# Optimization experiments

Hardware: AMD Instinct MI355X
Metric: run time of the kernel (lower is better)

The kernel has to match this reference:

```python
import jax, jax.numpy as jnp
import numpy as np

NEG_CLAMP = -100.0  # torch F.binary_cross_entropy clamps log terms at -100


def _ccl_labels(fg):
    """4-connectivity connected-component labeling of a [H,W] bool mask.
    Labels are assigned in raster-scan first-encounter order, matching
    scipy.ndimage.label with the default structure. Background = 0.
    Implemented as min-index label propagation to a fixed point: each
    component ends up tagged with the min flat index of its pixels (its
    first raster-scan pixel), then roots are ranked by cumsum to get 1..num.
    """
    H, W = fg.shape
    INF = H * W  # sentinel larger than any flat index
    idx = jnp.arange(INF, dtype=jnp.int32).reshape(H, W)
    init = jnp.where(fg, idx, INF)

    def step(x):
        up = jnp.concatenate([x[1:], jnp.full((1, W), INF, x.dtype)], axis=0)
        down = jnp.concatenate([jnp.full((1, W), INF, x.dtype), x[:-1]], axis=0)
        left = jnp.concatenate([x[:, 1:], jnp.full((H, 1), INF, x.dtype)], axis=1)
        right = jnp.concatenate([jnp.full((H, 1), INF, x.dtype), x[:, :-1]], axis=1)
        m = jnp.minimum(jnp.minimum(up, down), jnp.minimum(left, right))
        return jnp.where(fg, jnp.minimum(x, m), INF)

    def cond(carry):
        return carry[1]

    def body(carry):
        x, _ = carry
        nx = step(x)
        return nx, jnp.any(nx != x)

    x, _ = jax.lax.while_loop(cond, body, (init, jnp.array(True)))

    flat = x.reshape(-1)
    fgf = fg.reshape(-1)
    # a pixel is the root of its component iff its propagated tag == its own index
    is_root = fgf & (flat == jnp.arange(INF, dtype=jnp.int32))
    rank = jnp.cumsum(is_root.astype(jnp.int32))  # rank[r] = scipy label of root r
    labels = jnp.where(fgf, rank[jnp.clip(flat, 0, INF - 1)], 0)
    return labels.reshape(H, W)


def _target_map(fg):
    """Replicates: labels == labels.flatten()[1:].argmax() + 1 (faithful to source,
    including its quirky use of argmax position as the selected label value)."""
    labels = _ccl_labels(fg)
    lf = labels.reshape(-1)
    v = jnp.argmax(lf[1:]) + 1  # first occurrence of max, like numpy argmax
    return (labels == v).astype(jnp.float32)


def setup_inputs() -> dict:
    key = jax.random.key(0)
    pred = jax.random.uniform(key, (32, 1, 512, 512), dtype=jnp.float32)
    return {"pred": pred}


def reference(pred):
    fg = pred[:, 0] >= 0.5  # [N,H,W] bool
    target = jax.vmap(_target_map)(fg)[:, None]  # [N,1,H,W] float
    logp = jnp.maximum(jnp.log(pred), NEG_CLAMP)
    log1mp = jnp.maximum(jnp.log1p(-pred), NEG_CLAMP)
    return -jnp.mean(target * logp + (1.0 - target) * log1mp)
```

## Files before the change

### kernel.cpp

```cpp
#include <hip/hip_runtime.h>
#include <math.h>

#define IMG_W 512
#define IMG_H 512
#define HW (IMG_W * IMG_H)
#define LOGHW 18
#define NIMG 32
#define NTOT (NIMG * HW)
#define TILE 64
#define TPI 64
#define NTILE (NIMG * TPI)
#define CPI 64
#define NSCHUNK (NIMG * CPI)
#define VBORD ((8 - 1) * IMG_H)
#define BORD_PER_IMG (VBORD + (8 - 1) * IMG_W)
#define NBORD (NIMG * BORD_PER_IMG)

__device__ __forceinline__ void uf_unite(int* L, int a, int b) {
    while (true) {
        int p = ((volatile int*)L)[a];
        while (p != a) { a = p; p = ((volatile int*)L)[a]; }
        p = ((volatile int*)L)[b];
        while (p != b) { b = p; p = ((volatile int*)L)[b]; }
        if (a == b) return;
        if (a < b) { int t = a; a = b; b = t; }
        int old = atomicMin(&L[a], b);
        if (old == a) return;
        a = old;
    }
}

__global__ __launch_bounds__(256) void k_local(const float* __restrict__ pred,
                                               int* __restrict__ L,
                                               float* __restrict__ partials) {
    __shared__ int lab[TILE * TILE];
    __shared__ float sred[256];
    int tile = blockIdx.x;
    int img = tile >> 6;
    int t = tile & (TPI - 1);
    int ty = t >> 3, tx = t & 7;
    int baseLocal = (ty * TILE) * IMG_W + tx * TILE;
    const float* pi = pred + ((size_t)img << LOGHW);
    int* Li = L + ((size_t)img << LOGHW);
    int tid = threadIdx.x;
    int lane = tid & 63, wave = tid >> 6;

    float acc = 0.0f;
#pragma unroll
    for (int j = 0; j < 16; j++) {
        int row = wave + j * 4;
        float p = pi[baseLocal + row * IMG_W + lane];
        acc += fmaxf(log1pf(-p), -100.0f);
        bool fg = (p >= 0.5f);
        unsigned long long bal = __ballot(fg);
        unsigned long long starts = bal & ~(bal << 1);
        unsigned long long maskle =
            (lane == 63) ? ~0ULL : ((1ULL << (lane + 1)) - 1ULL);
        int lb = -1;
        if (fg) {
            unsigned long long pre = starts & maskle;
            int startLane = 63 - __builtin_clzll(pre);
            lb = row * TILE + startLane;
        }
        lab[row * TILE + lane] = lb;
    }
    __syncthreads();
#pragma unroll
    for (int j = 0; j < 16; j++) {
        int row = 1 + wave + j * 4;
        if (row > 63) break;
        int i = row * TILE + lane;
        bool c = (lab[i] >= 0) && (lab[i - TILE] >= 0);
        unsigned long long cb = __ballot(c);
        unsigned long long cs = cb & ~(cb << 1);
        if ((cs >> lane) & 1ULL) uf_unite(lab, i, i - TILE);
    }
    __syncthreads();
#pragma unroll
    for (int j = 0; j < 4; j++) {
        int i4 = (tid + j * 256) * 4;
        int ly = i4 >> 6, lx = i4 & 63;
        int4 o;
        int* op = (int*)&o;
#pragma unroll
        for (int k = 0; k < 4; k++) {
            int p = lab[i4 + k];
            if (p < 0) op[k] = -1;
            else {
                int x = i4 + k;
                while (p != x) { x = p; p = lab[x]; }
                op[k] = baseLocal + (x >> 6) * IMG_W + (x & 63);
            }
        }
        *(int4*)(Li + baseLocal + ly * IMG_W + lx) = o;
    }
    sred[tid] = acc;
    __syncthreads();
    for (int s = 128; s > 0; s >>= 1) {
        if (tid < s) sred[tid] += sred[tid + s];
        __syncthreads();
    }
    if (tid == 0) partials[blockIdx.x] = sred[0];
}

__global__ void k_border(int* __restrict__ L) {
    int gid = blockIdx.x * blockDim.x + threadIdx.x;
    if (gid >= NBORD) return;
    int img = gid / BORD_PER_IMG;
    int r = gid - img * BORD_PER_IMG;
    int* Li = L + ((size_t)img << LOGHW);
    int a, b;
    if (r < VBORD) {
        int k = r >> 9, y = r & 511;
        int x = k * TILE + (TILE - 1);
        a = y * IMG_W + x; b = a + 1;
    } else {
        int r2 = r - VBORD;
        int k = r2 >> 9, x = r2 & 511;
        int y = k * TILE + (TILE - 1);
        a = y * IMG_W + x; b = a + IMG_W;
    }
    if (Li[a] >= 0 && Li[b] >= 0) uf_unite(Li, a, b);
}

__global__ __launch_bounds__(256) void k_stats(const int* __restrict__ L,
                                               int* __restrict__ cntArr,
                                               int* __restrict__ maxArr,
                                               int* __restrict__ minArr) {
    __shared__ int s1[256], s2[256], s3[256];
    int chunk = blockIdx.x;
    int img = chunk >> 6;
    int baseL = (chunk & 63) * 4096;
    const int* Li = L + ((size_t)img << LOGHW);
    int t = threadIdx.x;
    int cnt = 0, mx = -1, mn = HW;
#pragma unroll
    for (int j = 0; j < 4; j++) {
        int off = baseL + (t + j * 256) * 4;
        int4 l4 = *(const int4*)(Li + off);
        const int* lp = (const int*)&l4;
#pragma unroll
        for (int k = 0; k < 4; k++) {
            int local = off + k;
            int p = lp[k];
            bool root = (p == local);
            cnt += root ? 1 : 0;
            if (root && local > mx) mx = local;
            if (p >= 0 && local >= 1 && local < mn) mn = local;
        }
    }
    s1[t] = cnt; s2[t] = mx; s3[t] = mn;
    __syncthreads();
    for (int s = 128; s > 0; s >>= 1) {
        if (t < s) {
            s1[t] += s1[t + s];
            s2[t] = max(s2[t], s2[t + s]);
            s3[t] = min(s3[t], s3[t + s]);
        }
        __syncthreads();
    }
    if (t == 0) { cntArr[chunk] = s1[0]; maxArr[chunk] = s2[0]; minArr[chunk] = s3[0]; }
}

__global__ __launch_bounds__(256) void k_rv(const int* __restrict__ cntArr,
                                            const int* __restrict__ maxArr,
                                            const int* __restrict__ minArr,
                                            const int* __restrict__ L,
                                            int* __restrict__ rv) {
    __shared__ int sc[256], sm[256], sn[256];
    __shared__ int sel_chunk, sel_base, result;
    int img = blockIdx.x, t = threadIdx.x;
    int cnt = (t < CPI) ? cntArr[img * CPI + t] : 0;
    sc[t] = cnt;
    sm[t] = (t < CPI) ? maxArr[img * CPI + t] : -1;
    sn[t] = (t < CPI) ? minArr[img * CPI + t] : HW;
    if (t == 0) result = -2;
    __syncthreads();
    for (int off = 1; off < 256; off <<= 1) {
        int v2 = (t >= off) ? sc[t - off] : 0;
        __syncthreads();
        sc[t] += v2;
        __syncthreads();
    }
    int num = sc[255];
    int inc = sc[t], exc = inc - cnt;
    for (int s = 128; s > 0; s >>= 1) {
        if (t < s) { sm[t] = max(sm[t], sm[t + s]); sn[t] = min(sn[t], sn[t + s]); }
        __syncthreads();
    }
    int last_root = sm[0], minFg = sn[0];
    int v;
    if (last_root >= 1) v = last_root;
    else if (last_root == 0) v = (minFg < HW) ? minFg : 1;
    else v = 1;
    if (v >= 1 && v <= num) {
        if (exc < v && v <= inc) { sel_chunk = t; sel_base = exc; }
        __syncthreads();
        int c = sel_chunk, base = sel_base;
        const int* Li = L + ((size_t)img << LOGHW);
        int baseL = c * 4096;
        int f[16];
        int sum = 0;
#pragma unroll
        for (int j = 0; j < 4; j++) {
            int off = baseL + t * 16 + j * 4;
            int4 l4 = *(const int4*)(Li + off);
            const int* lp = (const int*)&l4;
#pragma unroll
            for (int k = 0; k < 4; k++) {
                f[j * 4 + k] = (lp[k] == off + k) ? 1 : 0;
                sum += f[j * 4 + k];
            }
        }
        __syncthreads();
        sc[t] = sum;
        __syncthreads();
        for (int off = 1; off < 256; off <<= 1) {
            int v2 = (t >= off) ? sc[t - off] : 0;
            __syncthreads();
            sc[t] += v2;
            __syncthreads();
        }
        int exc2 = sc[t] - sum;
        int need = v - base;
        if (exc2 < need && need <= sc[t]) {
            int run = exc2;
#pragma unroll
            for (int k = 0; k < 16; k++) {
                run += f[k];
                if (run == need) { result = baseL + t * 16 + k; break; }
            }
        }
        __syncthreads();
    } else {
        __syncthreads();
    }
    if (t == 0) rv[img] = result;
}

__global__ __launch_bounds__(256) void k_loss(const float* __restrict__ pred,
                                              const int* __restrict__ L,
                                              const int* __restrict__ rvArr,
                                              float* __restrict__ partials2) {
    __shared__ float sred[256];
    int blk = blockIdx.x;
    int img = blk >> 6;
    int rvv = rvArr[img];
    if (rvv < 0) {
        if (threadIdx.x == 0) partials2[blk] = 0.0f;
        return;
    }
    const int* Li = L + ((size_t)img << LOGHW);
    int baseG = blk * 4096;
    int t = threadIdx.x;
    float acc = 0.0f;
#pragma unroll
    for (int j = 0; j < 4; j++) {
        int off = baseG + (t + j * 256) * 4;
        float4 p4 = *(const float4*)(pred + off);
        int4 l4 = *(const int4*)(L + off);
        const float* pp = (const float*)&p4;
        const int* lp = (const int*)&l4;
#pragma unroll
        for (int k = 0; k < 4; k++) {
            int p = lp[k];
            if (p < 0) continue;
            int x = p;
            int q = Li[x];
            while (q != x) { x = q; q = Li[x]; }
            if (x == rvv) {
                float pr = pp[k];
                float logp = fmaxf(logf(pr), -100.0f);
                float log1mp = fmaxf(log1pf(-pr), -100.0f);
                acc += logp - log1mp;
            }
        }
    }
    sred[t] = acc;
    __syncthreads();
    for (int s = 128; s > 0; s >>= 1) {
        if (t < s) sred[t] += sred[t + s];
        __syncthreads();
    }
    if (t == 0) partials2[blk] = sred[0];
}

__global__ __launch_bounds__(256) void k_final(const float* __restrict__ partials,
                                               const float* __restrict__ partials2,
                                               float* __restrict__ out) {
    __shared__ double s[256];
    int t = threadIdx.x;
    double acc = 0.0;
#pragma unroll
    for (int j = 0; j < 8; j++) {
        acc += (double)partials[t + j * 256] + (double)partials2[t + j * 256];
    }
    s[t] = acc;
    __syncthreads();
    for (int st = 128; st > 0; st >>= 1) {
        if (t < st) s[t] += s[t + st];
        __syncthreads();
    }
    if (t == 0) out[0] = (float)(-s[0] / (double)NTOT);
}

extern "C" void kernel_launch(void* const* d_in, const int* in_sizes, int n_in,
                              void* d_out, int out_size, void* d_ws, size_t ws_size,
                              hipStream_t stream) {
    const float* pred = (const float*)d_in[0];
    float* out = (float*)d_out;

    char* ws = (char*)d_ws;
    int* L = (int*)ws;
    int* cntArr = (int*)(ws + (size_t)NTOT * 4);
    int* maxArr = cntArr + NSCHUNK;
    int* minArr = maxArr + NSCHUNK;
    float* partials = (float*)(minArr + NSCHUNK);
    float* partials2 = partials + NTILE;
    int* rv = (int*)(partials2 + NTILE);

    dim3 b(256);
    k_local<<<dim3(NTILE), b, 0, stream>>>(pred, L, partials);
    k_border<<<dim3((NBORD + 255) / 256), b, 0, stream>>>(L);
    k_stats<<<dim3(NSCHUNK), b, 0, stream>>>(L, cntArr, maxArr, minArr);
    k_rv<<<dim3(NIMG), b, 0, stream>>>(cntArr, maxArr, minArr, L, rv);
    k_loss<<<dim3(NTILE), b, 0, stream>>>(pred, L, rv, partials2);
    k_final<<<1, b, 0, stream>>>(partials, partials2, out);
}
```

Baseline: 134.1 us.

## Fuse stats/rv and loss/final via last-block counters, widen local CCL blocks

Merges the per-image root-selection kernel into the stats kernel and the final reduction into the loss kernel, using atomic arrival counters so the last block of each group finishes the work. This removes two kernel launches. k_local now runs 1024 threads per tile and compresses paths in shared memory during root resolution. k_border uses a ballot so only run starts call union. The log terms use fast __logf(1-p) instead of log1pf, which can reduce accuracy near p=0.

```diff
diff --git a/kernel.cpp b/kernel.cpp
--- a/kernel.cpp
+++ b/kernel.cpp
@@ -16,6 +16,9 @@
 #define BORD_PER_IMG (VBORD + (8 - 1) * IMG_W)
 #define NBORD (NIMG * BORD_PER_IMG)
 
+#define AL_ACQ(p) __hip_atomic_load((p), __ATOMIC_ACQUIRE, __HIP_MEMORY_SCOPE_AGENT)
+#define AS_RLX(p, v) __hip_atomic_store((p), (v), __ATOMIC_RELAXED, __HIP_MEMORY_SCOPE_AGENT)
+
 __device__ __forceinline__ void uf_unite(int* L, int a, int b) {
     while (true) {
         int p = ((volatile int*)L)[a];
@@ -30,11 +33,12 @@
     }
 }
 
-__global__ __launch_bounds__(256) void k_local(const float* __restrict__ pred,
-                                               int* __restrict__ L,
-                                               float* __restrict__ partials) {
+__global__ __launch_bounds__(1024) void k_local(const float* __restrict__ pred,
+                                                int* __restrict__ L,
+                                                float* __restrict__ partials,
+                                                unsigned int* __restrict__ counters) {
     __shared__ int lab[TILE * TILE];
-    __shared__ float sred[256];
+    __shared__ float sred[1024];
     int tile = blockIdx.x;
     int img = tile >> 6;
     int t = tile & (TPI - 1);
@@ -47,10 +51,10 @@
 
     float acc = 0.0f;
 #pragma unroll
-    for (int j = 0; j < 16; j++) {
-        int row = wave + j * 4;
+    for (int j = 0; j < 4; j++) {
+        int row = wave + j * 16;
         float p = pi[baseLocal + row * IMG_W + lane];
-        acc += fmaxf(log1pf(-p), -100.0f);
+        acc += fmaxf(__logf(1.0f - p), -100.0f);
         bool fg = (p >= 0.5f);
         unsigned long long bal = __ballot(fg);
         unsigned long long starts = bal & ~(bal << 1);
@@ -59,16 +63,15 @@
         int lb = -1;
         if (fg) {
             unsigned long long pre = starts & maskle;
-            int startLane = 63 - __builtin_clzll(pre);
-            lb = row * TILE + startLane;
+            lb = row * TILE + (63 - __builtin_clzll(pre));
         }
         lab[row * TILE + lane] = lb;
     }
     __syncthreads();
 #pragma unroll
-    for (int j = 0; j < 16; j++) {
-        int row = 1 + wave + j * 4;
-        if (row > 63) break;
+    for (int j = 0; j < 4; j++) {
+        int row = wave + j * 16;
+        if (row == 0) continue;
         int i = row * TILE + lane;
         bool c = (lab[i] >= 0) && (lab[i - TILE] >= 0);
         unsigned long long cb = __ballot(c);
@@ -76,19 +79,23 @@
         if ((cs >> lane) & 1ULL) uf_unite(lab, i, i - TILE);
     }
     __syncthreads();
-#pragma unroll
-    for (int j = 0; j < 4; j++) {
-        int i4 = (tid + j * 256) * 4;
+    {
+        int i4 = tid * 4;
         int ly = i4 >> 6, lx = i4 & 63;
         int4 o;
         int* op = (int*)&o;
 #pragma unroll
         for (int k = 0; k < 4; k++) {
-            int p = lab[i4 + k];
+            int x = i4 + k;
+            int p = lab[x];
             if (p < 0) op[k] = -1;
             else {
-                int x = i4 + k;
-                while (p != x) { x = p; p = lab[x]; }
+                while (p != x) {
+                    int g = lab[p];
+                    lab[x] = g;
+                    x = g;
+                    p = lab[x];
+                }
                 op[k] = baseLocal + (x >> 6) * IMG_W + (x & 63);
             }
         }
@@ -96,16 +103,16 @@
     }
     sred[tid] = acc;
     __syncthreads();
-    for (int s = 128; s > 0; s >>= 1) {
+    for (int s = 512; s > 0; s >>= 1) {
         if (tid < s) sred[tid] += sred[tid + s];
         __syncthreads();
     }
     if (tid == 0) partials[blockIdx.x] = sred[0];
+    if (blockIdx.x == 0 && tid <= NIMG) counters[tid] = 0u;
 }
 
 __global__ void k_border(int* __restrict__ L) {
     int gid = blockIdx.x * blockDim.x + threadIdx.x;
-    if (gid >= NBORD) return;
     int img = gid / BORD_PER_IMG;
     int r = gid - img * BORD_PER_IMG;
     int* Li = L + ((size_t)img << LOGHW);
@@ -120,14 +127,21 @@
         int y = k * TILE + (TILE - 1);
         a = y * IMG_W + x; b = a + IMG_W;
     }
-    if (Li[a] >= 0 && Li[b] >= 0) uf_unite(Li, a, b);
-}
-
-__global__ __launch_bounds__(256) void k_stats(const int* __restrict__ L,
-                                               int* __restrict__ cntArr,
-                                               int* __restrict__ maxArr,
-                                               int* __restrict__ minArr) {
+    bool c = (Li[a] >= 0) && (Li[b] >= 0);
+    unsigned long long cb = __ballot(c);
+    unsigned long long cs = cb & ~(cb << 1);
+    if ((cs >> (threadIdx.x & 63)) & 1ULL) uf_unite(Li, a, b);
+}
+
+__global__ __launch_bounds__(256) void k_stats_rv(const int* __restrict__ L,
+                                                  int* __restrict__ cntArr,
+                                                  int* __restrict__ maxArr,
+                                                  int* __restrict__ minArr,
+                                                  unsigned int* __restrict__ counters,
+                                                  int* __restrict__ rv) {
     __shared__ int s1[256], s2[256], s3[256];
+    __shared__ int sel_chunk, sel_base, result;
+    __shared__ unsigned int oldc;
     int chunk = blockIdx.x;
     int img = chunk >> 6;
     int baseL = (chunk & 63) * 4096;
@@ -159,36 +173,35 @@
         }
         __syncthreads();
     }
-    if (t == 0) { cntArr[chunk] = s1[0]; maxArr[chunk] = s2[0]; minArr[chunk] = s3[0]; }
-}
-
-__global__ __launch_bounds__(256) void k_rv(const int* __restrict__ cntArr,
-                                            const int* __restrict__ maxArr,
-                                            const int* __restrict__ minArr,
-                                            const int* __restrict__ L,
-                                            int* __restrict__ rv) {
-    __shared__ int sc[256], sm[256], sn[256];
-    __shared__ int sel_chunk, sel_base, result;
-    int img = blockIdx.x, t = threadIdx.x;
-    int cnt = (t < CPI) ? cntArr[img * CPI + t] : 0;
-    sc[t] = cnt;
-    sm[t] = (t < CPI) ? maxArr[img * CPI + t] : -1;
-    sn[t] = (t < CPI) ? minArr[img * CPI + t] : HW;
+    if (t == 0) {
+        AS_RLX(&cntArr[chunk], s1[0]);
+        AS_RLX(&maxArr[chunk], s2[0]);
+        AS_RLX(&minArr[chunk], s3[0]);
+        oldc = __hip_atomic_fetch_add(&counters[img], 1u,
+                                      __ATOMIC_ACQ_REL, __HIP_MEMORY_SCOPE_AGENT);
+    }
+    __syncthreads();
+    if (oldc != CPI - 1) return;
+
+    int c0 = (t < CPI) ? AL_ACQ(&cntArr[img * CPI + t]) : 0;
+    s1[t] = c0;
+    s2[t] = (t < CPI) ? AL_ACQ(&maxArr[img * CPI + t]) : -1;
+    s3[t] = (t < CPI) ? AL_ACQ(&minArr[img * CPI + t]) : HW;
     if (t == 0) result = -2;
     __syncthreads();
     for (int off = 1; off < 256; off <<= 1) {
-        int v2 = (t >= off) ? sc[t - off] : 0;
-        __syncthreads();
-        sc[t] += v2;
-        __syncthreads();
-    }
-    int num = sc[255];
-    int inc = sc[t], exc = inc - cnt;
+        int v2 = (t >= off) ? s1[t - off] : 0;
+        __syncthreads();
+        s1[t] += v2;
+        __syncthreads();
+    }
+    int num = s1[255];
+    int inc = s1[t], exc = inc - c0;
     for (int s = 128; s > 0; s >>= 1) {
-        if (t < s) { sm[t] = max(sm[t], sm[t + s]); sn[t] = min(sn[t], sn[t + s]); }
-        __syncthreads();
-    }
-    int last_root = sm[0], minFg = sn[0];
+        if (t < s) { s2[t] = max(s2[t], s2[t + s]); s3[t] = min(s3[t], s3[t + s]); }
+        __syncthreads();
+    }
+    int last_root = s2[0], minFg = s3[0];
     int v;
     if (last_root >= 1) v = last_root;
     else if (last_root == 0) v = (minFg < HW) ? minFg : 1;
@@ -197,13 +210,12 @@
         if (exc < v && v <= inc) { sel_chunk = t; sel_base = exc; }
         __syncthreads();
         int c = sel_chunk, base = sel_base;
-        const int* Li = L + ((size_t)img << LOGHW);
-        int baseL = c * 4096;
+        int bL = c * 4096;
         int f[16];
         int sum = 0;
 #pragma unroll
         for (int j = 0; j < 4; j++) {
-            int off = baseL + t * 16 + j * 4;
+            int off = bL + t * 16 + j * 4;
             int4 l4 = *(const int4*)(Li + off);
             const int* lp = (const int*)&l4;
 #pragma unroll
@@ -213,22 +225,22 @@
             }
         }
         __syncthreads();
-        sc[t] = sum;
+        s1[t] = sum;
         __syncthreads();
         for (int off = 1; off < 256; off <<= 1) {
-            int v2 = (t >= off) ? sc[t - off] : 0;
+            int v2 = (t >= off) ? s1[t - off] : 0;
             __syncthreads();
-            sc[t] += v2;
+            s1[t] += v2;
             __syncthreads();
         }
-        int exc2 = sc[t] - sum;
+        int exc2 = s1[t] - sum;
         int need = v - base;
-        if (exc2 < need && need <= sc[t]) {
+        if (exc2 < need && need <= s1[t]) {
             int run = exc2;
 #pragma unroll
             for (int k = 0; k < 16; k++) {
                 run += f[k];
-                if (run == need) { result = baseL + t * 16 + k; break; }
+                if (run == need) { result = bL + t * 16 + k; break; }
             }
         }
         __syncthreads();
@@ -241,67 +253,71 @@
 __global__ __launch_bounds__(256) void k_loss(const float* __restrict__ pred,
                                               const int* __restrict__ L,
                                               const int* __restrict__ rvArr,
-                                              float* __restrict__ partials2) {
+                                              const float* __restrict__ partials,
+                                              float* __restrict__ partials2,
+                                              unsigned int* __restrict__ counters,
+                                              float* __restrict__ out) {
     __shared__ float sred[256];
+    __shared__ double sd[256];
+    __shared__ unsigned int oldc;
     int blk = blockIdx.x;
     int img = blk >> 6;
+    int t = threadIdx.x;
     int rvv = rvArr[img];
-    if (rvv < 0) {
-        if (threadIdx.x == 0) partials2[blk] = 0.0f;
-        return;
-    }
-    const int* Li = L + ((size_t)img << LOGHW);
-    int baseG = blk * 4096;
-    int t = threadIdx.x;
-    float acc = 0.0f;
-#pragma unroll
-    for (int j = 0; j < 4; j++) {
-        int off = baseG + (t + j * 256) * 4;
-        float4 p4 = *(const float4*)(pred + off);
-        int4 l4 = *(const int4*)(L + off);
-        const float* pp = (const float*)&p4;
-        const int* lp = (const int*)&l4;
-#pragma unroll
-        for (int k = 0; k < 4; k++) {
-            int p = lp[k];
-            if (p < 0) continue;
-            int x = p;
-            int q = Li[x];
-            while (q != x) { x = q; q = Li[x]; }
-            if (x == rvv) {
-                float pr = pp[k];
-                float logp = fmaxf(logf(pr), -100.0f);
-                float log1mp = fmaxf(log1pf(-pr), -100.0f);
-                acc += logp - log1mp;
+    float blocksum = 0.0f;
+    if (rvv >= 0) {
+        const int* Li = L + ((size_t)img << LOGHW);
+        int baseG = blk * 4096;
+        float acc = 0.0f;
+#pragma unroll
+        for (int j = 0; j < 4; j++) {
+            int off = baseG + (t + j * 256) * 4;
+            float4 p4 = *(const float4*)(pred + off);
+            int4 l4 = *(const int4*)(L + off);
+            const float* pp = (const float*)&p4;
+            const int* lp = (const int*)&l4;
+#pragma unroll
+            for (int k = 0; k < 4; k++) {
+                int p = lp[k];
+                if (p < 0) continue;
+                int x = p, q = Li[x];
+                while (q != x) { x = q; q = Li[x]; }
+                if (x == rvv) {
+                    float pr = pp[k];
+                    acc += fmaxf(__logf(pr), -100.0f)
+                         - fmaxf(__logf(1.0f - pr), -100.0f);
+                }
             }
         }
-    }
-    sred[t] = acc;
+        sred[t] = acc;
+        __syncthreads();
+        for (int s = 128; s > 0; s >>= 1) {
+            if (t < s) sred[t] += sred[t + s];
+            __syncthreads();
+        }
+        blocksum = sred[0];
+    }
+    if (t == 0) {
+        AS_RLX(&partials2[blk], blocksum);
+        oldc = __hip_atomic_fetch_add(&counters[NIMG], 1u,
+                                      __ATOMIC_ACQ_REL, __HIP_MEMORY_SCOPE_AGENT);
+    }
+    __syncthreads();
+    if (oldc != NTILE - 1) return;
+
+    double acc = 0.0;
+#pragma unroll
+    for (int j = 0; j < 8; j++) {
+        int idx = t + j * 256;
+        acc += (double)partials[idx] + (double)AL_ACQ(&partials2[idx]);
+    }
+    sd[t] = acc;
     __syncthreads();
     for (int s = 128; s > 0; s >>= 1) {
-        if (t < s) sred[t] += sred[t + s];
-        __syncthreads();
-    }
-    if (t == 0) partials2[blk] = sred[0];
-}
-
-__global__ __launch_bounds__(256) void k_final(const float* __restrict__ partials,
-                                               const float* __restrict__ partials2,
-                                               float* __restrict__ out) {
-    __shared__ double s[256];
-    int t = threadIdx.x;
-    double acc = 0.0;
-#pragma unroll
-    for (int j = 0; j < 8; j++) {
-        acc += (double)partials[t + j * 256] + (double)partials2[t + j * 256];
-    }
-    s[t] = acc;
-    __syncthreads();
-    for (int st = 128; st > 0; st >>= 1) {
-        if (t < st) s[t] += s[t + st];
-        __syncthreads();
-    }
-    if (t == 0) out[0] = (float)(-s[0] / (double)NTOT);
+        if (t < s) sd[t] += sd[t + s];
+        __syncthreads();
+    }
+    if (t == 0) out[0] = (float)(-sd[0] / (double)NTOT);
 }
 
 extern "C" void kernel_launch(void* const* d_in, const int* in_sizes, int n_in,
@@ -318,12 +334,12 @@
     float* partials = (float*)(minArr + NSCHUNK);
     float* partials2 = partials + NTILE;
     int* rv = (int*)(partials2 + NTILE);
-
-    dim3 b(256);
-    k_local<<<dim3(NTILE), b, 0, stream>>>(pred, L, partials);
-    k_border<<<dim3((NBORD + 255) / 256), b, 0, stream>>>(L);
-    k_stats<<<dim3(NSCHUNK), b, 0, stream>>>(L, cntArr, maxArr, minArr);
-    k_rv<<<dim3(NIMG), b, 0, stream>>>(cntArr, maxArr, minArr, L, rv);
-    k_loss<<<dim3(NTILE), b, 0, stream>>>(pred, L, rv, partials2);
-    k_final<<<1, b, 0, stream>>>(partials, partials2, out);
-}
+    unsigned int* counters = (unsigned int*)(rv + NIMG);
+
+    k_local<<<dim3(NTILE), dim3(1024), 0, stream>>>(pred, L, partials, counters);
+    k_border<<<dim3(NBORD / 256), dim3(256), 0, stream>>>(L);
+    k_stats_rv<<<dim3(NSCHUNK), dim3(256), 0, stream>>>(L, cntArr, maxArr, minArr,
+                                                        counters, rv);
+    k_loss<<<dim3(NTILE), dim3(256), 0, stream>>>(pred, L, rv, partials, partials2,
+                                                  counters, out);
+}
```

Result: slower. 223.9 us (+66.9%).

## Widen local CCL blocks, use fast logs, compress paths, dedupe border unions

Applied to the files above, without the earlier changes.

The local labeling kernel now runs with 512 threads per tile, so each wave handles fewer rows. Root-finding in shared memory gains path compression. Exact log1pf/logf calls are replaced by the __logf intrinsic on 1-p, which is cheaper but less accurate for p near 0 or 1. The border kernel drops its bounds check and uses a wave ballot so only the first pixel of each contiguous run of joinable pairs performs a union, cutting atomic traffic at the cost of relying on the run structure for correctness.

```diff
diff --git a/kernel.cpp b/kernel.cpp
--- a/kernel.cpp
+++ b/kernel.cpp
@@ -16,6 +16,7 @@
 #define BORD_PER_IMG (VBORD + (8 - 1) * IMG_W)
 #define NBORD (NIMG * BORD_PER_IMG)
 
+
 __device__ __forceinline__ void uf_unite(int* L, int a, int b) {
     while (true) {
         int p = ((volatile int*)L)[a];
@@ -30,11 +31,11 @@
     }
 }
 
-__global__ __launch_bounds__(256) void k_local(const float* __restrict__ pred,
+__global__ __launch_bounds__(512) void k_local(const float* __restrict__ pred,
                                                int* __restrict__ L,
                                                float* __restrict__ partials) {
     __shared__ int lab[TILE * TILE];
-    __shared__ float sred[256];
+    __shared__ float sred[512];
     int tile = blockIdx.x;
     int img = tile >> 6;
     int t = tile & (TPI - 1);
@@ -47,10 +48,10 @@
 
     float acc = 0.0f;
 #pragma unroll
-    for (int j = 0; j < 16; j++) {
-        int row = wave + j * 4;
+    for (int j = 0; j < 8; j++) {
+        int row = wave + j * 8;
         float p = pi[baseLocal + row * IMG_W + lane];
-        acc += fmaxf(log1pf(-p), -100.0f);
+        acc += fmaxf(__logf(1.0f - p), -100.0f);
         bool fg = (p >= 0.5f);
         unsigned long long bal = __ballot(fg);
         unsigned long long starts = bal & ~(bal << 1);
@@ -59,16 +60,15 @@
         int lb = -1;
         if (fg) {
             unsigned long long pre = starts & maskle;
-            int startLane = 63 - __builtin_clzll(pre);
-            lb = row * TILE + startLane;
+            lb = row * TILE + (63 - __builtin_clzll(pre));
         }
         lab[row * TILE + lane] = lb;
     }
     __syncthreads();
 #pragma unroll
-    for (int j = 0; j < 16; j++) {
-        int row = 1 + wave + j * 4;
-        if (row > 63) break;
+    for (int j = 0; j < 8; j++) {
+        int row = wave + j * 8;
+        if (row == 0) continue;
         int i = row * TILE + lane;
         bool c = (lab[i] >= 0) && (lab[i - TILE] >= 0);
         unsigned long long cb = __ballot(c);
@@ -77,18 +77,23 @@
     }
     __syncthreads();
 #pragma unroll
-    for (int j = 0; j < 4; j++) {
-        int i4 = (tid + j * 256) * 4;
+    for (int j = 0; j < 2; j++) {
+        int i4 = (tid + j * 512) * 4;
         int ly = i4 >> 6, lx = i4 & 63;
         int4 o;
         int* op = (int*)&o;
 #pragma unroll
         for (int k = 0; k < 4; k++) {
-            int p = lab[i4 + k];
+            int x = i4 + k;
+            int p = lab[x];
             if (p < 0) op[k] = -1;
             else {
-                int x = i4 + k;
-                while (p != x) { x = p; p = lab[x]; }
+                while (p != x) {
+                    int g = lab[p];
+                    lab[x] = g;
+                    x = g;
+                    p = lab[x];
+                }
                 op[k] = baseLocal + (x >> 6) * IMG_W + (x & 63);
             }
         }
@@ -96,7 +101,7 @@
     }
     sred[tid] = acc;
     __syncthreads();
-    for (int s = 128; s > 0; s >>= 1) {
+    for (int s = 256; s > 0; s >>= 1) {
         if (tid < s) sred[tid] += sred[tid + s];
         __syncthreads();
     }
@@ -105,7 +110,6 @@
 
 __global__ void k_border(int* __restrict__ L) {
     int gid = blockIdx.x * blockDim.x + threadIdx.x;
-    if (gid >= NBORD) return;
     int img = gid / BORD_PER_IMG;
     int r = gid - img * BORD_PER_IMG;
     int* Li = L + ((size_t)img << LOGHW);
@@ -120,7 +124,10 @@
         int y = k * TILE + (TILE - 1);
         a = y * IMG_W + x; b = a + IMG_W;
     }
-    if (Li[a] >= 0 && Li[b] >= 0) uf_unite(Li, a, b);
+    bool c = (Li[a] >= 0) && (Li[b] >= 0);
+    unsigned long long cb = __ballot(c);
+    unsigned long long cs = cb & ~(cb << 1);
+    if ((cs >> (threadIdx.x & 63)) & 1ULL) uf_unite(Li, a, b);
 }
 
 __global__ __launch_bounds__(256) void k_stats(const int* __restrict__ L,
@@ -245,14 +252,14 @@
     __shared__ float sred[256];
     int blk = blockIdx.x;
     int img = blk >> 6;
+    int t = threadIdx.x;
     int rvv = rvArr[img];
     if (rvv < 0) {
-        if (threadIdx.x == 0) partials2[blk] = 0.0f;
+        if (t == 0) partials2[blk] = 0.0f;
         return;
     }
     const int* Li = L + ((size_t)img << LOGHW);
     int baseG = blk * 4096;
-    int t = threadIdx.x;
     float acc = 0.0f;
 #pragma unroll
     for (int j = 0; j < 4; j++) {
@@ -265,14 +272,12 @@
         for (int k = 0; k < 4; k++) {
             int p = lp[k];
             if (p < 0) continue;
-            int x = p;
-            int q = Li[x];
+            int x = p, q = Li[x];
             while (q != x) { x = q; q = Li[x]; }
             if (x == rvv) {
                 float pr = pp[k];
-                float logp = fmaxf(logf(pr), -100.0f);
-                float log1mp = fmaxf(log1pf(-pr), -100.0f);
-                acc += logp - log1mp;
+                acc += fmaxf(__logf(pr), -100.0f)
+                     - fmaxf(__logf(1.0f - pr), -100.0f);
             }
         }
     }
@@ -293,7 +298,8 @@
     double acc = 0.0;
 #pragma unroll
     for (int j = 0; j < 8; j++) {
-        acc += (double)partials[t + j * 256] + (double)partials2[t + j * 256];
+        int idx = t + j * 256;
+        acc += (double)partials[idx] + (double)partials2[idx];
     }
     s[t] = acc;
     __syncthreads();
@@ -317,13 +323,12 @@
     int* minArr = maxArr + NSCHUNK;
     float* partials = (float*)(minArr + NSCHUNK);
     float* partials2 = partials + NTILE;
-    int* rv = (int*)(partials2 + NTILE);
-
-    dim3 b(256);
-    k_local<<<dim3(NTILE), b, 0, stream>>>(pred, L, partials);
-    k_border<<<dim3((NBORD + 255) / 256), b, 0, stream>>>(L);
-    k_stats<<<dim3(NSCHUNK), b, 0, stream>>>(L, cntArr, maxArr, minArr);
-    k_rv<<<dim3(NIMG), b, 0, stream>>>(cntArr, maxArr, minArr, L, rv);
-    k_loss<<<dim3(NTILE), b, 0, stream>>>(pred, L, rv, partials2);
-    k_final<<<1, b, 0, stream>>>(partials, partials2, out);
-}
+    int* rv = (int*)(partials2 + NSCHUNK);
+
+    k_local<<<dim3(NTILE), dim3(512), 0, stream>>>(pred, L, partials);
+    k_border<<<dim3(NBORD / 256), dim3(256), 0, stream>>>(L);
+    k_stats<<<dim3(NSCHUNK), dim3(256), 0, stream>>>(L, cntArr, maxArr, minArr);
+    k_rv<<<dim3(NIMG), dim3(256), 0, stream>>>(cntArr, maxArr, minArr, L, rv);
+    k_loss<<<dim3(NSCHUNK), dim3(256), 0, stream>>>(pred, L, rv, partials2);
+    k_final<<<1, dim3(256), 0, stream>>>(partials, partials2, out);
+}
```

After: 123.6 us. 7.9% less time.
